# Optimization experiments

Hardware: AMD Instinct MI355X
Metric: run time of the kernel (lower is better)

## Reference

```python
import jax, jax.numpy as jnp
import numpy as np

B, T, D, H = 4, 2048, 1024, 16
DH = D // H

def setup_inputs() -> dict:
    key = jax.random.key(0)
    ks = jax.random.split(key, 8)
    scale = 1.0 / np.sqrt(D)
    return {
        "q": jax.random.normal(ks[0], (B, T, D), dtype=jnp.float32),
        "k": jax.random.normal(ks[1], (B, T, D), dtype=jnp.float32),
        "v": jax.random.normal(ks[2], (B, T, D), dtype=jnp.float32),
        "wq": jax.random.normal(ks[3], (D, D), dtype=jnp.float32) * scale,
        "wk": jax.random.normal(ks[4], (D, D), dtype=jnp.float32) * scale,
        "wv": jax.random.normal(ks[5], (D, D), dtype=jnp.float32) * scale,
        "wo": jax.random.normal(ks[6], (D, D), dtype=jnp.float32) * scale,
        "mask": jnp.tril(jnp.ones((T, T), dtype=bool)),  # causal [Tq,Tk]
    }

def reference(q, k, v, wq, wk, wv, wo, mask):
    Bq, Tq, C = q.shape
    Tk = k.shape[1]
    # nn.Linear(bias=False): y = x @ W.T, W is [out,in]
    qh = (q @ wq.T).reshape(Bq, Tq, H, DH).transpose(0, 2, 1, 3)  # [B,H,Tq,DH]
    kh = (k @ wk.T).reshape(Bq, Tk, H, DH).transpose(0, 2, 1, 3)
    vh = (v @ wv.T).reshape(Bq, Tk, H, DH).transpose(0, 2, 1, 3)
    att = jnp.einsum("bhqd,bhkd->bhqk", qh, kh) / np.sqrt(DH)
    att = jnp.where(mask[None, None, :, :], att, -jnp.inf)
    att = jax.nn.softmax(att, axis=-1)
    out = jnp.einsum("bhqk,bhkd->bhqd", att, vh)
    out = out.transpose(0, 2, 1, 3).reshape(Bq, Tq, C)
    return out @ wo.T
```

## Files before the change

kernel.cpp:

```cpp
#include <hip/hip_runtime.h>
#include <hip/hip_bf16.h>

typedef short bf16x8 __attribute__((ext_vector_type(8)));
typedef float f32x4 __attribute__((ext_vector_type(4)));
typedef float f32x16 __attribute__((ext_vector_type(16)));

#define N_B 4
#define N_T 2048
#define N_D 1024
#define N_H 16
#define N_DH 64

#define Q_SCALE 0.18033688011112042f

__device__ __forceinline__ unsigned short f2bf(float f) {
  union { float f; unsigned int u; } c; c.f = f;
  unsigned int u = c.u;
  return (unsigned short)((u + 0x7FFFu + ((u >> 16) & 1u)) >> 16);
}

__device__ __forceinline__ unsigned cvtpk_bf16(float lo, float hi) {
  unsigned r;
  asm("v_cvt_pk_bf16_f32 %0, %1, %2" : "=v"(r) : "v"(lo), "v"(hi));
  return r;
}

__device__ __forceinline__ void gll16(const unsigned short* g, unsigned short* l) {
  __builtin_amdgcn_global_load_lds(
      (const __attribute__((address_space(1))) unsigned int*)(const void*)g,
      (__attribute__((address_space(3))) unsigned int*)(void*)l, 16, 0, 0);
}

__global__ void cast_all(const float* __restrict__ wq, const float* __restrict__ wk,
                         const float* __restrict__ wv, const float* __restrict__ wo,
                         const float* __restrict__ q, const float* __restrict__ k,
                         const float* __restrict__ v,
                         unsigned short* __restrict__ ws) {
  const int z = blockIdx.z;
  const float* srcs[7] = {wq, wk, wv, wo, q, k, v};
  const int size = (z < 4) ? (N_D * N_D) : (N_B * N_T * N_D);
  const size_t off = (z < 4) ? (size_t)z * (N_D * N_D)
                             : (size_t)4 * (N_D * N_D) + (size_t)(z - 4) * (N_B * N_T * N_D);
  const int i = (blockIdx.x * 256 + threadIdx.x) * 8;
  if (i >= size) return;
  const float* src = srcs[z];
  float4 a = *(const float4*)(src + i);
  float4 b = *(const float4*)(src + i + 4);
  bf16x8 p;
  p[0] = (short)f2bf(a.x); p[1] = (short)f2bf(a.y);
  p[2] = (short)f2bf(a.z); p[3] = (short)f2bf(a.w);
  p[4] = (short)f2bf(b.x); p[5] = (short)f2bf(b.y);
  p[6] = (short)f2bf(b.z); p[7] = (short)f2bf(b.w);
  *(bf16x8*)(ws + off + i) = p;
}

__launch_bounds__(256, 2)
__global__ void proj_qkv(const unsigned short* __restrict__ qb,
                         const unsigned short* __restrict__ kb,
                         const unsigned short* __restrict__ vb,
                         const unsigned short* __restrict__ wq,
                         const unsigned short* __restrict__ wk,
                         const unsigned short* __restrict__ wv,
                         unsigned short* __restrict__ qh,
                         unsigned short* __restrict__ kh,
                         unsigned short* __restrict__ vt) {
  const int z = blockIdx.z;
  const unsigned short* X = (z == 0) ? qb : (z == 1) ? kb : vb;
  const unsigned short* W = (z == 0) ? wq : (z == 1) ? wk : wv;
  unsigned short* O = (z == 0) ? qh : (z == 1) ? kh : vt;

  __shared__ unsigned short lds_a[128 * 64];
  __shared__ unsigned short lds_b[128 * 64];

  const int tid = threadIdx.x;
  const int wave = tid >> 6, lane = tid & 63;
  const int wm = wave >> 1, wn = wave & 1;
  const int lr = lane & 15, lg = lane >> 4;
  const int orig = blockIdx.y * 8 + blockIdx.x;
  const int swz = (orig & 7) * 64 + (orig >> 3);
  const int m0 = (swz >> 3) * 128, n0 = (swz & 7) * 128;
  const int sw = (lr & 7) << 4;

  f32x4 acc[4][4] = {};

  for (int k0 = 0; k0 < N_D; k0 += 64) {
    __syncthreads();
#pragma unroll
    for (int it = 0; it < 4; ++it) {
      int c = it * 256 + tid;
      int row = c >> 3;
      int sb = ((c & 7) * 16) ^ ((row & 7) << 4);
      gll16(&X[(size_t)(m0 + row) * N_D + k0 + (sb >> 1)], &lds_a[c * 8]);
      gll16(&W[(size_t)(n0 + row) * N_D + k0 + (sb >> 1)], &lds_b[c * 8]);
    }
    __syncthreads();

#pragma unroll
    for (int kk = 0; kk < 2; ++kk) {
      bf16x8 af[4], bfr[4];
      const int cb = (lg * 16 + kk * 64);
#pragma unroll
      for (int m = 0; m < 4; ++m)
        af[m] = *(bf16x8*)&lds_a[(wm * 64 + m * 16 + lr) * 64 + ((cb ^ sw) >> 1)];
#pragma unroll
      for (int n = 0; n < 4; ++n)
        bfr[n] = *(bf16x8*)&lds_b[(wn * 64 + n * 16 + lr) * 64 + ((cb ^ sw) >> 1)];
#pragma unroll
      for (int m = 0; m < 4; ++m)
#pragma unroll
        for (int n = 0; n < 4; ++n)
          acc[m][n] = __builtin_amdgcn_mfma_f32_16x16x32_bf16(af[m], bfr[n], acc[m][n], 0, 0, 0);
    }
  }

  const float osc = (z == 0) ? Q_SCALE : 1.0f;
#pragma unroll
  for (int m = 0; m < 4; ++m)
#pragma unroll
    for (int n = 0; n < 4; ++n)
#pragma unroll
      for (int r = 0; r < 4; ++r) {
        int row = m0 + wm * 64 + m * 16 + lg * 4 + r;
        int col = n0 + wn * 64 + n * 16 + lr;
        int b = row >> 11, t = row & (N_T - 1);
        int hh = col >> 6, dh = col & 63;
        unsigned short val = f2bf(acc[m][n][r] * osc);
        if (z < 2)
          O[(((size_t)(b * N_H + hh)) * N_T + t) * N_DH + dh] = val;
        else
          O[(((size_t)(b * N_H + hh)) * N_DH + dh) * N_T + t] = val;
      }
}

__launch_bounds__(256, 2)
__global__ void proj_out(const unsigned short* __restrict__ A,
                         const unsigned short* __restrict__ W,
                         float* __restrict__ out) {
  __shared__ unsigned short lds_a[128 * 64];
  __shared__ unsigned short lds_b[128 * 64];

  const int tid = threadIdx.x;
  const int wave = tid >> 6, lane = tid & 63;
  const int wm = wave >> 1, wn = wave & 1;
  const int lr = lane & 15, lg = lane >> 4;
  const int orig = blockIdx.y * 8 + blockIdx.x;
  const int swz = (orig & 7) * 64 + (orig >> 3);
  const int m0 = (swz >> 3) * 128, n0 = (swz & 7) * 128;
  const int sw = (lr & 7) << 4;

  f32x4 acc[4][4] = {};

  for (int k0 = 0; k0 < N_D; k0 += 64) {
    __syncthreads();
#pragma unroll
    for (int it = 0; it < 4; ++it) {
      int c = it * 256 + tid;
      int row = c >> 3;
      int sb = ((c & 7) * 16) ^ ((row & 7) << 4);
      gll16(&A[(size_t)(m0 + row) * N_D + k0 + (sb >> 1)], &lds_a[c * 8]);
      gll16(&W[(size_t)(n0 + row) * N_D + k0 + (sb >> 1)], &lds_b[c * 8]);
    }
    __syncthreads();

#pragma unroll
    for (int kk = 0; kk < 2; ++kk) {
      bf16x8 af[4], bfr[4];
      const int cb = (lg * 16 + kk * 64);
#pragma unroll
      for (int m = 0; m < 4; ++m)
        af[m] = *(bf16x8*)&lds_a[(wm * 64 + m * 16 + lr) * 64 + ((cb ^ sw) >> 1)];
#pragma unroll
      for (int n = 0; n < 4; ++n)
        bfr[n] = *(bf16x8*)&lds_b[(wn * 64 + n * 16 + lr) * 64 + ((cb ^ sw) >> 1)];
#pragma unroll
      for (int m = 0; m < 4; ++m)
#pragma unroll
        for (int n = 0; n < 4; ++n)
          acc[m][n] = __builtin_amdgcn_mfma_f32_16x16x32_bf16(af[m], bfr[n], acc[m][n], 0, 0, 0);
    }
  }

#pragma unroll
  for (int m = 0; m < 4; ++m)
#pragma unroll
    for (int n = 0; n < 4; ++n)
#pragma unroll
      for (int r = 0; r < 4; ++r) {
        int row = m0 + wm * 64 + m * 16 + lg * 4 + r;
        int col = n0 + wn * 64 + n * 16 + lr;
        out[(size_t)row * N_D + col] = acc[m][n][r];
      }
}

__launch_bounds__(256, 2)
__global__ void attn(const unsigned short* __restrict__ qh,
                     const unsigned short* __restrict__ kh,
                     const unsigned short* __restrict__ vt,
                     unsigned short* __restrict__ att) {
  __shared__ unsigned short k_lds[2][64 * 64];
  __shared__ unsigned short v_lds[2][64 * 64];

  const int tid = threadIdx.x;
  const int wave = tid >> 6, lane = tid & 63;
  const int l31 = lane & 31, hi = lane >> 5;
  const int bh = blockIdx.y;
  const size_t base = (size_t)bh * N_T * N_DH;
  const unsigned short* Q = qh + base;
  const unsigned short* K = kh + base;
  const unsigned short* V = vt + base;
  const int b = bh >> 4, h = bh & 15;
  const int swr = (l31 & 7) << 4;

  bf16x8 ones;
#pragma unroll
  for (int j = 0; j < 8; ++j) ones[j] = (short)0x3F80;

  auto stage = [&](int buf, int kb2) {
    const int kk0 = kb2 * 64;
#pragma unroll
    for (int it = 0; it < 2; ++it) {
      int c = it * 256 + tid;
      int row = c >> 3;
      int sb = ((c & 7) * 16) ^ ((row & 7) << 4);
      gll16(&K[(size_t)(kk0 + row) * N_DH + (sb >> 1)], &k_lds[buf][c * 8]);
      gll16(&V[(size_t)row * N_T + kk0 + (sb >> 1)], &v_lds[buf][c * 8]);
    }
  };

  for (int half = 0; half < 2; ++half) {
    const int qt = half ? (15 - (int)blockIdx.x) : (int)blockIdx.x;
    const int q0 = qt * 128;
    const int q0w = q0 + wave * 32;

    bf16x8 qf[4];
#pragma unroll
    for (int i = 0; i < 4; ++i)
      qf[i] = *(const bf16x8*)&Q[(size_t)(q0w + l31) * N_DH + i * 16 + hi * 8];

    float m_r = -INFINITY;
    f32x16 l_acc = {};
    f32x16 o0 = {}, o1 = {};

    const int nkb = 2 * qt + 2;

    __syncthreads();
    stage(0, 0);

    for (int kb = 0; kb < nkb; ++kb) {
      const int cur = kb & 1;
      __syncthreads();
      if (kb + 1 < nkb) stage(cur ^ 1, kb + 1);

      const unsigned short* kt_ = k_lds[cur];
      const unsigned short* vt_ = v_lds[cur];

#pragma unroll
      for (int ks = 0; ks < 2; ++ks) {
        const int kgb = kb * 64 + ks * 32;
        if (kgb > q0w + 31) continue;

        f32x16 s = {};
        __builtin_amdgcn_s_setprio(1);
#pragma unroll
        for (int i = 0; i < 4; ++i) {
          bf16x8 kf = *(const bf16x8*)&kt_[(ks * 32 + l31) * 64 +
                                           (((i * 32 + hi * 16) ^ swr) >> 1)];
          s = __builtin_amdgcn_mfma_f32_32x32x16_bf16(kf, qf[i], s, 0, 0, 0);
        }
        __builtin_amdgcn_s_setprio(0);

        if (kgb == q0w) {
#pragma unroll
          for (int j = 0; j < 16; ++j)
            if ((j & 3) + 8 * (j >> 2) + 4 * hi > l31) s[j] = -1e30f;
        }

        float mx = s[0];
#pragma unroll
        for (int j = 1; j < 16; ++j) mx = fmaxf(mx, s[j]);
        mx = fmaxf(mx, __shfl_xor(mx, 32));
        if (__any(mx > m_r + 8.0f)) {
          float mn = fmaxf(m_r, mx);
          float al = exp2f(m_r - mn);
          m_r = mn;
#pragma unroll
          for (int j = 0; j < 16; ++j) {
            float aj = __shfl(al, (j & 3) + 8 * (j >> 2) + 4 * hi);
            o0[j] *= aj; o1[j] *= aj; l_acc[j] *= aj;
          }
        }

#pragma unroll
        for (int j = 0; j < 16; ++j) s[j] = exp2f(s[j] - m_r);

        unsigned t01 = cvtpk_bf16(s[0], s[1]),   t45 = cvtpk_bf16(s[4], s[5]);
        unsigned t23 = cvtpk_bf16(s[2], s[3]),   t67 = cvtpk_bf16(s[6], s[7]);
        unsigned u01 = cvtpk_bf16(s[8], s[9]),   u45 = cvtpk_bf16(s[12], s[13]);
        unsigned u23 = cvtpk_bf16(s[10], s[11]), u67 = cvtpk_bf16(s[14], s[15]);
        unsigned x01 = __shfl_xor(t01, 32), x45 = __shfl_xor(t45, 32);
        unsigned x23 = __shfl_xor(t23, 32), x67 = __shfl_xor(t67, 32);
        unsigned y01 = __shfl_xor(u01, 32), y45 = __shfl_xor(u45, 32);
        unsigned y23 = __shfl_xor(u23, 32), y67 = __shfl_xor(u67, 32);
        union { unsigned u[4]; bf16x8 v; } pa0, pa1;
        pa0.u[0] = hi ? x45 : t01;  pa0.u[1] = hi ? x67 : t23;
        pa0.u[2] = hi ? t45 : x01;  pa0.u[3] = hi ? t67 : x23;
        pa1.u[0] = hi ? y45 : u01;  pa1.u[1] = hi ? y67 : u23;
        pa1.u[2] = hi ? u45 : y01;  pa1.u[3] = hi ? u67 : y23;

        const int c0 = ((ks * 64 + hi * 16) ^ swr) >> 1;
        const int c1 = ((ks * 64 + 32 + hi * 16) ^ swr) >> 1;
        bf16x8 v00 = *(const bf16x8*)&vt_[l31 * 64 + c0];
        bf16x8 v01 = *(const bf16x8*)&vt_[(32 + l31) * 64 + c0];
        bf16x8 v10 = *(const bf16x8*)&vt_[l31 * 64 + c1];
        bf16x8 v11 = *(const bf16x8*)&vt_[(32 + l31) * 64 + c1];

        __builtin_amdgcn_s_setprio(1);
        o0 = __builtin_amdgcn_mfma_f32_32x32x16_bf16(pa0.v, v00, o0, 0, 0, 0);
        o1 = __builtin_amdgcn_mfma_f32_32x32x16_bf16(pa0.v, v01, o1, 0, 0, 0);
        o0 = __builtin_amdgcn_mfma_f32_32x32x16_bf16(pa1.v, v10, o0, 0, 0, 0);
        o1 = __builtin_amdgcn_mfma_f32_32x32x16_bf16(pa1.v, v11, o1, 0, 0, 0);
        l_acc = __builtin_amdgcn_mfma_f32_32x32x16_bf16(pa0.v, ones, l_acc, 0, 0, 0);
        l_acc = __builtin_amdgcn_mfma_f32_32x32x16_bf16(pa1.v, ones, l_acc, 0, 0, 0);
        __builtin_amdgcn_s_setprio(0);
      }
    }

#pragma unroll
    for (int j = 0; j < 16; ++j) {
      float inv = 1.0f / l_acc[j];
      int t = q0w + (j & 3) + 8 * (j >> 2) + 4 * hi;
      size_t rowb = ((size_t)(b * N_T + t)) * N_D + h * 64 + l31;
      att[rowb]      = f2bf(o0[j] * inv);
      att[rowb + 32] = f2bf(o1[j] * inv);
    }
  }
}

extern "C" void kernel_launch(void* const* d_in, const int* in_sizes, int n_in,
                              void* d_out, int out_size, void* d_ws, size_t ws_size,
                              hipStream_t stream) {
  (void)in_sizes; (void)n_in; (void)out_size; (void)ws_size;
  const float* q  = (const float*)d_in[0];
  const float* k  = (const float*)d_in[1];
  const float* v  = (const float*)d_in[2];
  const float* wq = (const float*)d_in[3];
  const float* wk = (const float*)d_in[4];
  const float* wv = (const float*)d_in[5];
  const float* wo = (const float*)d_in[6];
  float* out = (float*)d_out;

  unsigned short* ws = (unsigned short*)d_ws;
  const size_t W_ELEMS = (size_t)N_D * N_D;
  const size_t T_ELEMS = (size_t)N_B * N_T * N_D;
  unsigned short* wqb = ws;
  unsigned short* wkb = wqb + W_ELEMS;
  unsigned short* wvb = wkb + W_ELEMS;
  unsigned short* wob = wvb + W_ELEMS;
  unsigned short* qb  = wob + W_ELEMS;
  unsigned short* kb  = qb + T_ELEMS;
  unsigned short* vb  = kb + T_ELEMS;
  unsigned short* qhb = vb + T_ELEMS;
  unsigned short* khb = qhb + T_ELEMS;
  unsigned short* vtb = khb + T_ELEMS;
  unsigned short* att = qb;

  cast_all<<<dim3(4096, 1, 7), 256, 0, stream>>>(wq, wk, wv, wo, q, k, v, ws);
  proj_qkv<<<dim3(8, 64, 3), 256, 0, stream>>>(qb, kb, vb, wqb, wkb, wvb, qhb, khb, vtb);
  attn<<<dim3(8, N_B * N_H), 256, 0, stream>>>(qhb, khb, vtb, att);
  proj_out<<<dim3(8, 64), 256, 0, stream>>>(att, wob, out);
}
```

Baseline: 210.3 us.

## Process both 32-key sub-blocks together with one softmax rescale per block

The attention inner loop now computes QK^T scores for both 32-key halves of a 64-key LDS tile up front, then does a single max reduction and one conditional rescale of the accumulators per tile instead of per half. This halves the shuffle and max-check overhead and exposes more independent MFMA work for the scheduler to interleave. Block indices are also remapped so that consecutive workgroups share heads (blocks of 8 heads across 8 query-pair positions), aiming at better L2 locality for K/V. The cost is higher register pressure from holding two score tiles live, which could hurt occupancy under the 2-blocks-per-CU launch bound.

Result: faster. 205.0 us (-2.5%).

```diff
diff --git a/kernel.cpp b/kernel.cpp
--- a/kernel.cpp
+++ b/kernel.cpp
@@ -203,7 +203,9 @@
   const int tid = threadIdx.x;
   const int wave = tid >> 6, lane = tid & 63;
   const int l31 = lane & 31, hi = lane >> 5;
-  const int bh = blockIdx.y;
+  const int L = (int)blockIdx.x + (int)blockIdx.y * 8;
+  const int bh = (L & 7) | ((L >> 6) << 3);
+  const int px = (L >> 3) & 7;
   const size_t base = (size_t)bh * N_T * N_DH;
   const unsigned short* Q = qh + base;
   const unsigned short* K = kh + base;
@@ -228,7 +230,7 @@
   };
 
   for (int half = 0; half < 2; ++half) {
-    const int qt = half ? (15 - (int)blockIdx.x) : (int)blockIdx.x;
+    const int qt = half ? (15 - px) : px;
     const int q0 = qt * 128;
     const int q0w = q0 + wave * 32;
 
@@ -254,49 +256,69 @@
       const unsigned short* kt_ = k_lds[cur];
       const unsigned short* vt_ = v_lds[cur];
 
-#pragma unroll
-      for (int ks = 0; ks < 2; ++ks) {
-        const int kgb = kb * 64 + ks * 32;
-        if (kgb > q0w + 31) continue;
-
-        f32x16 s = {};
-        __builtin_amdgcn_s_setprio(1);
+      const int kgb0 = kb * 64;
+      const int kgb1 = kb * 64 + 32;
+      if (kgb0 > q0w + 31) continue;
+      const bool a1 = (kgb1 <= q0w + 31);
+
+      f32x16 s0 = {}, s1 = {};
+      __builtin_amdgcn_s_setprio(1);
+#pragma unroll
+      for (int i = 0; i < 4; ++i) {
+        bf16x8 kf = *(const bf16x8*)&kt_[l31 * 64 + (((i * 32 + hi * 16) ^ swr) >> 1)];
+        s0 = __builtin_amdgcn_mfma_f32_32x32x16_bf16(kf, qf[i], s0, 0, 0, 0);
+      }
+      if (a1) {
 #pragma unroll
         for (int i = 0; i < 4; ++i) {
-          bf16x8 kf = *(const bf16x8*)&kt_[(ks * 32 + l31) * 64 +
-                                           (((i * 32 + hi * 16) ^ swr) >> 1)];
-          s = __builtin_amdgcn_mfma_f32_32x32x16_bf16(kf, qf[i], s, 0, 0, 0);
+          bf16x8 kf = *(const bf16x8*)&kt_[(32 + l31) * 64 + (((i * 32 + hi * 16) ^ swr) >> 1)];
+          s1 = __builtin_amdgcn_mfma_f32_32x32x16_bf16(kf, qf[i], s1, 0, 0, 0);
         }
-        __builtin_amdgcn_s_setprio(0);
-
-        if (kgb == q0w) {
-#pragma unroll
-          for (int j = 0; j < 16; ++j)
-            if ((j & 3) + 8 * (j >> 2) + 4 * hi > l31) s[j] = -1e30f;
+      }
+      __builtin_amdgcn_s_setprio(0);
+
+      if (kgb0 == q0w) {
+#pragma unroll
+        for (int j = 0; j < 16; ++j)
+          if ((j & 3) + 8 * (j >> 2) + 4 * hi > l31) s0[j] = -1e30f;
+      }
+      if (a1 && kgb1 == q0w) {
+#pragma unroll
+        for (int j = 0; j < 16; ++j)
+          if ((j & 3) + 8 * (j >> 2) + 4 * hi > l31) s1[j] = -1e30f;
+      }
+
+      float mx = s0[0];
+#pragma unroll
+      for (int j = 1; j < 16; ++j) mx = fmaxf(mx, s0[j]);
+      if (a1) {
+#pragma unroll
+        for (int j = 0; j < 16; ++j) mx = fmaxf(mx, s1[j]);
+      }
+      mx = fmaxf(mx, __shfl_xor(mx, 32));
+      if (__any(mx > m_r + 8.0f)) {
+        float mn = fmaxf(m_r, mx);
+        float al = exp2f(m_r - mn);
+        m_r = mn;
+#pragma unroll
+        for (int j = 0; j < 16; ++j) {
+          float aj = __shfl(al, (j & 3) + 8 * (j >> 2) + 4 * hi);
+          o0[j] *= aj; o1[j] *= aj; l_acc[j] *= aj;
         }
-
-        float mx = s[0];
-#pragma unroll
-        for (int j = 1; j < 16; ++j) mx = fmaxf(mx, s[j]);
-        mx = fmaxf(mx, __shfl_xor(mx, 32));
-        if (__any(mx > m_r + 8.0f)) {
-          float mn = fmaxf(m_r, mx);
-          float al = exp2f(m_r - mn);
-          m_r = mn;
-#pragma unroll
-          for (int j = 0; j < 16; ++j) {
-            float aj = __shfl(al, (j & 3) + 8 * (j >> 2) + 4 * hi);
-            o0[j] *= aj; o1[j] *= aj; l_acc[j] *= aj;
-          }
-        }
-
-#pragma unroll
-        for (int j = 0; j < 16; ++j) s[j] = exp2f(s[j] - m_r);
-
-        unsigned t01 = cvtpk_bf16(s[0], s[1]),   t45 = cvtpk_bf16(s[4], s[5]);
-        unsigned t23 = cvtpk_bf16(s[2], s[3]),   t67 = cvtpk_bf16(s[6], s[7]);
-        unsigned u01 = cvtpk_bf16(s[8], s[9]),   u45 = cvtpk_bf16(s[12], s[13]);
-        unsigned u23 = cvtpk_bf16(s[10], s[11]), u67 = cvtpk_bf16(s[14], s[15]);
+      }
+
+#pragma unroll
+      for (int j = 0; j < 16; ++j) s0[j] = exp2f(s0[j] - m_r);
+      if (a1) {
+#pragma unroll
+        for (int j = 0; j < 16; ++j) s1[j] = exp2f(s1[j] - m_r);
+      }
+
+      {
+        unsigned t01 = cvtpk_bf16(s0[0], s0[1]),   t45 = cvtpk_bf16(s0[4], s0[5]);
+        unsigned t23 = cvtpk_bf16(s0[2], s0[3]),   t67 = cvtpk_bf16(s0[6], s0[7]);
+        unsigned u01 = cvtpk_bf16(s0[8], s0[9]),   u45 = cvtpk_bf16(s0[12], s0[13]);
+        unsigned u23 = cvtpk_bf16(s0[10], s0[11]), u67 = cvtpk_bf16(s0[14], s0[15]);
         unsigned x01 = __shfl_xor(t01, 32), x45 = __shfl_xor(t45, 32);
         unsigned x23 = __shfl_xor(t23, 32), x67 = __shfl_xor(t67, 32);
         unsigned y01 = __shfl_xor(u01, 32), y45 = __shfl_xor(u45, 32);
@@ -307,8 +329,8 @@
         pa1.u[0] = hi ? y45 : u01;  pa1.u[1] = hi ? y67 : u23;
         pa1.u[2] = hi ? u45 : y01;  pa1.u[3] = hi ? u67 : y23;
 
-        const int c0 = ((ks * 64 + hi * 16) ^ swr) >> 1;
-        const int c1 = ((ks * 64 + 32 + hi * 16) ^ swr) >> 1;
+        const int c0 = ((hi * 16) ^ swr) >> 1;
+        const int c1 = ((32 + hi * 16) ^ swr) >> 1;
         bf16x8 v00 = *(const bf16x8*)&vt_[l31 * 64 + c0];
         bf16x8 v01 = *(const bf16x8*)&vt_[(32 + l31) * 64 + c0];
         bf16x8 v10 = *(const bf16x8*)&vt_[l31 * 64 + c1];
@@ -321,6 +343,38 @@
         o1 = __builtin_amdgcn_mfma_f32_32x32x16_bf16(pa1.v, v11, o1, 0, 0, 0);
         l_acc = __builtin_amdgcn_mfma_f32_32x32x16_bf16(pa0.v, ones, l_acc, 0, 0, 0);
         l_acc = __builtin_amdgcn_mfma_f32_32x32x16_bf16(pa1.v, ones, l_acc, 0, 0, 0);
+        __builtin_amdgcn_s_setprio(0);
+      }
+
+      if (a1) {
+        unsigned t01 = cvtpk_bf16(s1[0], s1[1]),   t45 = cvtpk_bf16(s1[4], s1[5]);
+        unsigned t23 = cvtpk_bf16(s1[2], s1[3]),   t67 = cvtpk_bf16(s1[6], s1[7]);
+        unsigned u01 = cvtpk_bf16(s1[8], s1[9]),   u45 = cvtpk_bf16(s1[12], s1[13]);
+        unsigned u23 = cvtpk_bf16(s1[10], s1[11]), u67 = cvtpk_bf16(s1[14], s1[15]);
+        unsigned x01 = __shfl_xor(t01, 32), x45 = __shfl_xor(t45, 32);
+        unsigned x23 = __shfl_xor(t23, 32), x67 = __shfl_xor(t67, 32);
+        unsigned y01 = __shfl_xor(u01, 32), y45 = __shfl_xor(u45, 32);
+        unsigned y23 = __shfl_xor(u23, 32), y67 = __shfl_xor(u67, 32);
+        union { unsigned u[4]; bf16x8 v; } pb0, pb1;
+        pb0.u[0] = hi ? x45 : t01;  pb0.u[1] = hi ? x67 : t23;
+        pb0.u[2] = hi ? t45 : x01;  pb0.u[3] = hi ? t67 : x23;
+        pb1.u[0] = hi ? y45 : u01;  pb1.u[1] = hi ? y67 : u23;
+        pb1.u[2] = hi ? u45 : y01;  pb1.u[3] = hi ? u67 : y23;
+
+        const int c0 = ((64 + hi * 16) ^ swr) >> 1;
+        const int c1 = ((96 + hi * 16) ^ swr) >> 1;
+        bf16x8 v00 = *(const bf16x8*)&vt_[l31 * 64 + c0];
+        bf16x8 v01 = *(const bf16x8*)&vt_[(32 + l31) * 64 + c0];
+        bf16x8 v10 = *(const bf16x8*)&vt_[l31 * 64 + c1];
+        bf16x8 v11 = *(const bf16x8*)&vt_[(32 + l31) * 64 + c1];
+
+        __builtin_amdgcn_s_setprio(1);
+        o0 = __builtin_amdgcn_mfma_f32_32x32x16_bf16(pb0.v, v00, o0, 0, 0, 0);
+        o1 = __builtin_amdgcn_mfma_f32_32x32x16_bf16(pb0.v, v01, o1, 0, 0, 0);
+        o0 = __builtin_amdgcn_mfma_f32_32x32x16_bf16(pb1.v, v10, o0, 0, 0, 0);
+        o1 = __builtin_amdgcn_mfma_f32_32x32x16_bf16(pb1.v, v11, o1, 0, 0, 0);
+        l_acc = __builtin_amdgcn_mfma_f32_32x32x16_bf16(pb0.v, ones, l_acc, 0, 0, 0);
+        l_acc = __builtin_amdgcn_mfma_f32_32x32x16_bf16(pb1.v, ones, l_acc, 0, 0, 0);
         __builtin_amdgcn_s_setprio(0);
       }
     }
```
